# Kernel optimization log

Hardware: AMD Instinct MI355X
Metric: run time of the kernel (lower is better)

Reference implementation:

```python
import jax, jax.numpy as jnp
import numpy as np

D_MODEL = 512
D_INNER = 1024      # expand * d_model
NHEADS = 16         # d_inner // headdim, headdim = d_model // num_heads = 64
HEADDIM = 64
DSTATE = 64
DCONV = 4           # window_size
DFF = 2048
B, LM, LT = 16, 1024, 512


def _rmsnorm(x, eps=1e-6):
    return x * jax.lax.rsqrt(jnp.mean(x * x, axis=-1, keepdims=True) + eps)


def setup_inputs():
    key = jax.random.key(0)
    ks = jax.random.split(key, 10)
    conv_dim = D_INNER + 2 * DSTATE
    d_in_proj = 2 * D_INNER + 2 * DSTATE + NHEADS
    return {
        'tgt': jax.random.normal(ks[0], (B, LT, D_MODEL), jnp.float32),
        'memory': jax.random.normal(ks[1], (B, LM, D_MODEL), jnp.float32),
        'mem_mask': jnp.ones((B, LM), jnp.float32),
        'tgt_mask': jnp.ones((B, LT), jnp.float32),
        'in_proj_w': jax.random.normal(ks[2], (d_in_proj, D_MODEL), jnp.float32) * 0.02,
        'conv_w': jax.random.normal(ks[3], (conv_dim, DCONV), jnp.float32) * 0.2,
        'conv_b': jnp.zeros((conv_dim,), jnp.float32),
        'dt_bias': jax.random.uniform(ks[4], (NHEADS,), jnp.float32, -4.0, -2.0),
        'A_log': jnp.log(jax.random.uniform(ks[5], (NHEADS,), jnp.float32, 1.0, 16.0)),
        'D': jnp.ones((NHEADS,), jnp.float32),
        'norm_w': jnp.ones((D_INNER,), jnp.float32),
        'out_proj_w': jax.random.normal(ks[6], (D_MODEL, D_INNER), jnp.float32) * 0.02,
        'fc1_w': jax.random.normal(ks[7], (DFF, D_MODEL), jnp.float32) * 0.02,
        'fc1_b': jnp.zeros((DFF,), jnp.float32),
        'fc2_w': jax.random.normal(ks[8], (D_MODEL, DFF), jnp.float32) * 0.02,
        'fc2_b': jnp.zeros((D_MODEL,), jnp.float32),
    }


def _mamba2(u, in_proj_w, conv_w, conv_b, dt_bias, A_log, D, norm_w, out_proj_w):
    # u: (B, L, d_model) -- Mamba2-style selective scan (causal, ngroups=1)
    b, L, _ = u.shape
    zxbcdt = jnp.einsum('bld,ed->ble', u, in_proj_w)  # (B,L,2192)
    z = zxbcdt[..., :D_INNER]
    xBC = zxbcdt[..., D_INNER:D_INNER + D_INNER + 2 * DSTATE]
    dt = zxbcdt[..., -NHEADS:]

    # causal depthwise conv1d, kernel = DCONV, then swish
    xBC_pad = jnp.pad(xBC, ((0, 0), (DCONV - 1, 0), (0, 0)))
    conv = conv_b
    conv = sum(conv_w[:, k] * xBC_pad[:, k:k + L] for k in range(DCONV)) + conv_b
    xBC = jax.nn.silu(conv)

    x = xBC[..., :D_INNER].reshape(b, L, NHEADS, HEADDIM)   # (B,L,H,P)
    Bm = xBC[..., D_INNER:D_INNER + DSTATE]                  # (B,L,N)
    Cm = xBC[..., D_INNER + DSTATE:]                         # (B,L,N)

    dt = jax.nn.softplus(dt + dt_bias)                       # (B,L,H)
    A = -jnp.exp(A_log)                                      # (H,)
    a = jnp.exp(dt * A)                                      # (B,L,H) decay

    def step(h, inputs):
        a_t, dt_t, x_t, B_t, C_t = inputs
        # h: (B,H,P,N)
        h = a_t[:, :, None, None] * h + (dt_t[:, :, None] * x_t)[..., None] * B_t[:, None, None, :]
        y = jnp.einsum('bhpn,bn->bhp', h, C_t)
        return h, y

    h0 = jnp.zeros((b, NHEADS, HEADDIM, DSTATE), u.dtype)
    xs = (jnp.moveaxis(a, 1, 0), jnp.moveaxis(dt, 1, 0), jnp.moveaxis(x, 1, 0),
          jnp.moveaxis(Bm, 1, 0), jnp.moveaxis(Cm, 1, 0))
    _, ys = jax.lax.scan(step, h0, xs)                       # (L,B,H,P)
    y = jnp.moveaxis(ys, 0, 1) + D[None, None, :, None] * x  # skip term
    y = y.reshape(b, L, D_INNER)

    # gated RMSNorm + out_proj
    y = y * jax.nn.silu(z)
    y = _rmsnorm(y, 1e-5) * norm_w
    return jnp.einsum('ble,de->bld', y, out_proj_w)


def _forward(tgt, memory, mem_mask, tgt_mask, in_proj_w, conv_w, conv_b, dt_bias,
             A_log, D, norm_w, out_proj_w, fc1_w, fc1_b, fc2_w, fc2_b):
    tgt = tgt * tgt_mask[..., None]
    tgt1 = _rmsnorm(tgt)
    memory = memory * mem_mask[..., None]
    u = jnp.concatenate([memory, tgt1], axis=1)
    mask = jnp.concatenate([mem_mask, tgt_mask], axis=1)
    u = u * mask[..., None]
    tgt2 = _mamba2(u, in_proj_w, conv_w, conv_b, dt_bias, A_log, D, norm_w, out_proj_w)
    tgt2 = tgt2[:, -tgt1.shape[1]:]
    tgt = tgt + tgt2  # dropout = identity (eval)
    tgt1 = _rmsnorm(tgt)
    h = jax.nn.gelu(jnp.einsum('bld,fd->blf', tgt1, fc1_w) + fc1_b, approximate=False)
    tgt2 = jnp.einsum('blf,df->bld', h, fc2_w) + fc2_b
    return tgt + tgt2


def reference(tgt, memory, mem_mask, tgt_mask, in_proj_w, conv_w, conv_b, dt_bias,
              A_log, D, norm_w, out_proj_w, fc1_w, fc1_b, fc2_w, fc2_b):
    return _forward(tgt, memory, mem_mask, tgt_mask, in_proj_w, conv_w, conv_b, dt_bias,
                    A_log, D, norm_w, out_proj_w, fc1_w, fc1_b, fc2_w, fc2_b)
```

## Files before the change

kernel.cpp:

```cpp
#include <hip/hip_runtime.h>
#include <cstddef>

#define BB 16
#define LMM 1024
#define LTT 512
#define LL 1536
#define DMODEL 512
#define DINNER 1024
#define NH 16
#define DIPROJ 2192
#define DFF2 2048

typedef __bf16 bf16_t;
typedef bf16_t bf16x2 __attribute__((ext_vector_type(2)));
typedef bf16_t bf16x4 __attribute__((ext_vector_type(4)));
typedef bf16_t bf16x8 __attribute__((ext_vector_type(8)));
typedef float f32x4 __attribute__((ext_vector_type(4)));

typedef __attribute__((address_space(3))) void lds_void;
typedef const __attribute__((address_space(1))) void glb_void;

__device__ __forceinline__ void gload16(const void* g, void* l) {
  __builtin_amdgcn_global_load_lds((glb_void*)g, (lds_void*)l, 16, 0, 0);
}

__device__ inline float block_sum(float v, float* sbuf) {
#pragma unroll
  for (int off = 32; off > 0; off >>= 1) v += __shfl_xor(v, off, 64);
  int w = threadIdx.x >> 6;
  if ((threadIdx.x & 63) == 0) sbuf[w] = v;
  __syncthreads();
  return sbuf[0] + sbuf[1] + sbuf[2] + sbuf[3];
}

__global__ __launch_bounds__(256)
void cvt_w(const float* __restrict__ src, bf16_t* __restrict__ dst, int n)
{
  int i = (blockIdx.x * 256 + threadIdx.x) * 4;
  if (i < n) {
    float4 v = *(const float4*)&src[i];
    bf16x4 o;
    o[0] = (bf16_t)v.x; o[1] = (bf16_t)v.y; o[2] = (bf16_t)v.z; o[3] = (bf16_t)v.w;
    *(bf16x4*)&dst[i] = o;
  }
}

__global__ __launch_bounds__(256)
void prep_u(const float* __restrict__ tgt, const float* __restrict__ memory,
            const float* __restrict__ mem_mask, const float* __restrict__ tgt_mask,
            bf16_t* __restrict__ u, float* __restrict__ tgtm)
{
  __shared__ float sbuf[4];
  const int row = blockIdx.x;
  const int b = row / LL;
  const int t = row - b * LL;
  const int tid = threadIdx.x;
  if (t < LMM) {
    float m = mem_mask[b * LMM + t];
    float s = m * m;
    const float* src = memory + ((size_t)b * LMM + t) * DMODEL;
    float2 v = *(const float2*)&src[tid * 2];
    bf16x2 o; o[0] = (bf16_t)(v.x * s); o[1] = (bf16_t)(v.y * s);
    *(bf16x2*)&u[(size_t)row * DMODEL + tid * 2] = o;
  } else {
    const int tt = t - LMM;
    float mk = tgt_mask[b * LTT + tt];
    const float* src = tgt + ((size_t)b * LTT + tt) * DMODEL;
    float2 v = *(const float2*)&src[tid * 2];
    v.x *= mk; v.y *= mk;
    *(float2*)&tgtm[((size_t)b * LTT + tt) * DMODEL + tid * 2] = v;
    float ss = block_sum(v.x * v.x + v.y * v.y, sbuf);
    float inv = rsqrtf(ss * (1.0f / 512.0f) + 1e-6f) * mk;
    bf16x2 o; o[0] = (bf16_t)(v.x * inv); o[1] = (bf16_t)(v.y * inv);
    *(bf16x2*)&u[(size_t)row * DMODEL + tid * 2] = o;
  }
}

template<int EPI>
__global__ __launch_bounds__(256)
void gemm_abf(const bf16_t* __restrict__ A, const bf16_t* __restrict__ W,
              int M, int N, int K,
              float* __restrict__ Cf, bf16_t* __restrict__ Cb,
              const float* __restrict__ bias, const float* __restrict__ res,
              bf16_t* __restrict__ zbuf, bf16_t* __restrict__ xbc,
              float* __restrict__ dts, float* __restrict__ labuf,
              const float* __restrict__ dt_bias, const float* __restrict__ A_log)
{
  const int m0 = blockIdx.y * 128;
  const int n0 = blockIdx.x * 128;
  int bq = 0, tbase = 0;
  if (EPI == 4) {
    bq = m0 / LL; tbase = m0 - bq * LL;
    if (n0 + 128 <= DINNER && tbase < LMM) return;
  }
  __shared__ __align__(16) bf16_t As[128 * 64];
  __shared__ __align__(16) bf16_t Bs[128 * 64];
  const int tid = threadIdx.x;
  const int lane = tid & 63;
  const int wid = tid >> 6;
  const int wr = (wid >> 1) * 64, wc = (wid & 1) * 64;
  const int r = lane & 15;
  const int g = lane >> 4;
  const int r7 = r & 7;
  const int lrow = lane >> 3;
  const int sslot = (lane & 7) ^ lrow;

  int arow[4], brow[4];
#pragma unroll
  for (int ci = 0; ci < 4; ++ci) {
    int tr = wid * 32 + ci * 8 + lrow;
    arow[ci] = m0 + tr;
    int bn = n0 + tr;
    brow[ci] = bn < N ? bn : N - 1;
  }

  f32x4 acc[4][4];
#pragma unroll
  for (int m = 0; m < 4; ++m)
#pragma unroll
    for (int n = 0; n < 4; ++n) acc[m][n] = (f32x4){0.f, 0.f, 0.f, 0.f};

  for (int kt = 0; kt < K; kt += 64) {
#pragma unroll
    for (int ci = 0; ci < 4; ++ci) {
      int chunk = wid * 4 + ci;
      gload16(A + (size_t)arow[ci] * K + kt + sslot * 8, &As[chunk * 512]);
      gload16(W + (size_t)brow[ci] * K + kt + sslot * 8, &Bs[chunk * 512]);
    }
    __syncthreads();
#pragma unroll
    for (int c = 0; c < 2; ++c) {
      bf16x8 af[4], bfr[4];
#pragma unroll
      for (int m = 0; m < 4; ++m) {
        int row = wr + m * 16 + r;
        af[m] = *(const bf16x8*)&As[row * 64 + (((c * 4 + g) ^ r7) * 8)];
      }
#pragma unroll
      for (int n = 0; n < 4; ++n) {
        int row = wc + n * 16 + r;
        bfr[n] = *(const bf16x8*)&Bs[row * 64 + (((c * 4 + g) ^ r7) * 8)];
      }
#pragma unroll
      for (int m = 0; m < 4; ++m)
#pragma unroll
        for (int n = 0; n < 4; ++n)
          acc[m][n] = __builtin_amdgcn_mfma_f32_16x16x32_bf16(af[m], bfr[n], acc[m][n], 0, 0, 0);
    }
    __syncthreads();
  }

#pragma unroll
  for (int m = 0; m < 4; ++m) {
#pragma unroll
    for (int n = 0; n < 4; ++n) {
      int gcol = n0 + wc + n * 16 + r;
      if (gcol >= N) continue;
#pragma unroll
      for (int j = 0; j < 4; ++j) {
        float v = acc[m][n][j];
        if (EPI == 4) {
          int t = tbase + wr + m * 16 + g * 4 + j;
          if (gcol < DINNER) {
            zbuf[(((size_t)(bq * LTT + t - LMM)) << 10) + gcol] = (bf16_t)v;
          } else if (gcol < DINNER + 1152) {
            xbc[(size_t)(bq * LL + t) * 1152 + (gcol - DINNER)] = (bf16_t)v;
          } else {
            int h = gcol - 2176;
            float raw = v + dt_bias[h];
            float d = raw > 20.f ? raw : log1pf(expf(raw));
            size_t ix = (size_t)(bq * LL + t) * 16 + h;
            dts[ix] = d;
            labuf[ix] = -expf(A_log[h]) * d;
          }
        } else {
          int grow = m0 + wr + m * 16 + g * 4 + j;
          if (EPI == 1) {
            v += bias[gcol];
            v = 0.5f * v * (1.f + erff(v * 0.70710678f));
            Cb[(size_t)grow * N + gcol] = (bf16_t)v;
          } else if (EPI == 2) {
            v += bias[gcol] + res[(size_t)grow * N + gcol];
            Cf[(size_t)grow * N + gcol] = v;
          } else {
            v += res[(size_t)grow * N + gcol];
            Cf[(size_t)grow * N + gcol] = v;
          }
        }
      }
    }
  }
}

__global__ __launch_bounds__(256)
void sbc_k(const bf16_t* __restrict__ xbc, const float* __restrict__ cw,
           const float* __restrict__ cb, bf16_t* __restrict__ BtG,
           bf16_t* __restrict__ Sg, bf16_t* __restrict__ CcG)
{
  __shared__ __align__(16) bf16_t rawBC[132 * 128];
  __shared__ __align__(16) bf16_t CB[128 * 128];
  __shared__ float wls[128 * 4];
  __shared__ float bls[128];
  const int c = blockIdx.x, b = blockIdx.y;
  const int t0 = c * 128;
  const int tid = threadIdx.x, lane = tid & 63, wid = tid >> 6;
  const int r = lane & 15, g = lane >> 4;

  if (tid < 128) {
    int gch = 1024 + tid;
#pragma unroll
    for (int k = 0; k < 4; ++k) wls[tid * 4 + k] = cw[gch * 4 + k];
    bls[tid] = cb[gch];
  }
#pragma unroll
  for (int ci = 0; ci < 9; ++ci) {
    int chunk = ci * 4 + wid;
    if (chunk < 33) {
      int F = chunk * 1024 + lane * 16;
      int row = F >> 8, off = F & 255;
      gload16(xbc + (size_t)(b * LL + t0 - 3 + row) * 1152 + 1024 + off / 2,
              &rawBC[chunk * 512]);
    }
  }
  __syncthreads();
  if (c == 0 && tid < 48) {
    bf16x8 z; 
#pragma unroll
    for (int j = 0; j < 8; ++j) z[j] = (bf16_t)0.f;
    *(bf16x8*)&rawBC[tid * 8] = z;
  }
  __syncthreads();
#pragma unroll 2
  for (int it = 0; it < 64; ++it) {
    int o = tid + it * 256;
    int t = o >> 7, ch = o & 127;
    float a0 = bls[ch];
#pragma unroll
    for (int kk = 0; kk < 4; ++kk)
      a0 = fmaf(wls[ch * 4 + kk], (float)rawBC[(t + kk) * 128 + ch], a0);
    float sv = a0 / (1.f + expf(-a0));
    int slot = ch >> 3;
    int swslot = (slot & 8) | ((slot & 7) ^ (t & 7));
    CB[t * 128 + swslot * 8 + (ch & 7)] = (bf16_t)sv;
    if (c >= 8 && ch >= 64) {
      int n = ch - 64;
      CcG[(((size_t)(b * 4 + (c - 8)) * 128 + t)) * 64 + (((n >> 3) ^ (t & 7)) << 3) + (n & 7)] = (bf16_t)sv;
    }
  }
  __syncthreads();
  {
    int n = tid & 63, tb = tid >> 6;
#pragma unroll
    for (int s8 = 0; s8 < 4; ++s8) {
      int ts = tb * 32 + s8 * 8;
      bf16x8 v;
#pragma unroll
      for (int e = 0; e < 8; ++e) {
        int t = ts + e;
        int slot = (n >> 3) ^ (t & 7);
        v[e] = CB[t * 128 + slot * 8 + (n & 7)];
      }
      *(bf16x8*)&BtG[((size_t)(b * 12 + c) * 64 + n) * 128 + ((((ts >> 3) ^ (n & 7))) << 3)] = v;
    }
  }
  if (c >= 8) {
    f32x4 sacc[2][8];
#pragma unroll
    for (int tt = 0; tt < 2; ++tt)
#pragma unroll
      for (int ct = 0; ct < 8; ++ct) sacc[tt][ct] = (f32x4){0.f, 0.f, 0.f, 0.f};
    const int ctn = 2 * wid + 2;
#pragma unroll
    for (int kk = 0; kk < 2; ++kk) {
      bf16x8 ca[2];
#pragma unroll
      for (int tt = 0; tt < 2; ++tt) {
        int trow = wid * 32 + tt * 16 + r;
        int slot = (64 + kk * 32 + g * 8) >> 3;
        int sw = (slot & 8) | ((slot & 7) ^ (trow & 7));
        ca[tt] = *(const bf16x8*)&CB[trow * 128 + sw * 8];
      }
#pragma unroll
      for (int ct = 0; ct < 8; ++ct) {
        if (ct < ctn) {
          int taur = ct * 16 + r;
          int sw = ((kk * 4 + g) ^ (taur & 7));
          bf16x8 bb = *(const bf16x8*)&CB[taur * 128 + sw * 8];
          sacc[0][ct] = __builtin_amdgcn_mfma_f32_16x16x32_bf16(ca[0], bb, sacc[0][ct], 0, 0, 0);
          sacc[1][ct] = __builtin_amdgcn_mfma_f32_16x16x32_bf16(ca[1], bb, sacc[1][ct], 0, 0, 0);
        }
      }
    }
    size_t sbase = (size_t)(b * 4 + (c - 8)) * 16384;
#pragma unroll
    for (int tt = 0; tt < 2; ++tt)
#pragma unroll
      for (int ct = 0; ct < 8; ++ct) {
        if (ct < ctn) {
#pragma unroll
          for (int j = 0; j < 4; ++j) {
            int ta = wid * 32 + tt * 16 + g * 4 + j;
            int tau = ct * 16 + r;
            Sg[sbase + ta * 128 + (tau ^ ((ta & 7) << 3))] = (bf16_t)sacc[tt][ct][j];
          }
        }
      }
  }
}

__global__ __launch_bounds__(256)
void ssd_hend(const bf16_t* __restrict__ xbc, const float* __restrict__ dts,
              const float* __restrict__ labuf, const float* __restrict__ cw,
              const float* __restrict__ cb, const bf16_t* __restrict__ BtG,
              bf16_t* __restrict__ hend, float* __restrict__ Lacum,
              float* __restrict__ Ak)
{
  __shared__ __align__(16) bf16_t rawX[136 * 64];
  __shared__ __align__(16) bf16_t Xt[64 * 128];
  __shared__ __align__(16) bf16_t Bt[64 * 128];
  __shared__ float wv[128];
  __shared__ float wls[64 * 4];
  __shared__ float bls[64];
  const int c = blockIdx.x;
  const int bh = blockIdx.y;
  const int b = bh >> 4, h = bh & 15;
  const int t0 = c * 128;
  const int tid = threadIdx.x, lane = tid & 63, wid = tid >> 6;
  const int r = lane & 15, g = lane >> 4;

  if (tid < 64) {
    int gch = h * 64 + tid;
#pragma unroll
    for (int k = 0; k < 4; ++k) wls[tid * 4 + k] = cw[gch * 4 + k];
    bls[tid] = cb[gch];
  }
#pragma unroll
  for (int ci = 0; ci < 5; ++ci) {
    int chunk = ci * 4 + wid;
    if (chunk < 17) {
      int F = chunk * 1024 + lane * 16;
      int row = F >> 7, off = F & 127;
      gload16(xbc + (size_t)(b * LL + t0 - 3 + row) * 1152 + h * 64 + off / 2,
              &rawX[chunk * 512]);
    }
  }
#pragma unroll
  for (int ci = 0; ci < 4; ++ci) {
    int chunk = ci * 4 + wid;
    int F = chunk * 1024 + lane * 16;
    gload16(BtG + (size_t)(b * 12 + c) * 8192 + F / 2, &Bt[chunk * 512]);
  }
  __syncthreads();
  if (c == 0 && tid < 24) {
    bf16x8 z;
#pragma unroll
    for (int j = 0; j < 8; ++j) z[j] = (bf16_t)0.f;
    *(bf16x8*)&rawX[tid * 8] = z;
  }
  if (tid < 64) {
    float v0 = labuf[(size_t)(b * LL + t0 + tid) * 16 + h];
    float v1 = labuf[(size_t)(b * LL + t0 + 64 + tid) * 16 + h];
    float d0 = dts[(size_t)(b * LL + t0 + tid) * 16 + h];
    float d1 = dts[(size_t)(b * LL + t0 + 64 + tid) * 16 + h];
#pragma unroll
    for (int d = 1; d < 64; d <<= 1) { float t_ = __shfl(v0, tid - d, 64); if (tid >= d) v0 += t_; }
    float T0 = __shfl(v0, 63, 64);
#pragma unroll
    for (int d = 1; d < 64; d <<= 1) { float t_ = __shfl(v1, tid - d, 64); if (tid >= d) v1 += t_; }
    v1 += T0;
    float Ls = __shfl(v1, 63, 64);
    wv[tid] = expf(Ls - v0) * d0; wv[64 + tid] = expf(Ls - v1) * d1;
    Lacum[(size_t)(bh * 12 + c) * 128 + tid] = v0;
    Lacum[(size_t)(bh * 12 + c) * 128 + 64 + tid] = v1;
    if (tid == 0) Ak[bh * 12 + c] = expf(Ls);
  }
  __syncthreads();
  {
    int p = tid & 63, tb = (tid >> 6) * 32;
    float w0 = wls[p * 4], w1 = wls[p * 4 + 1], w2 = wls[p * 4 + 2], w3 = wls[p * 4 + 3];
    float bb0 = bls[p];
    int sw = (p & 7) << 3;
#pragma unroll
    for (int i8 = 0; i8 < 4; ++i8) {
      bf16x8 ov;
#pragma unroll
      for (int e = 0; e < 8; ++e) {
        int t = tb + i8 * 8 + e;
        float a0 = bb0;
        a0 = fmaf(w0, (float)rawX[(t + 0) * 64 + p], a0);
        a0 = fmaf(w1, (float)rawX[(t + 1) * 64 + p], a0);
        a0 = fmaf(w2, (float)rawX[(t + 2) * 64 + p], a0);
        a0 = fmaf(w3, (float)rawX[(t + 3) * 64 + p], a0);
        ov[e] = (bf16_t)(a0 / (1.f + expf(-a0)));
      }
      *(bf16x8*)&Xt[p * 128 + ((tb + i8 * 8) ^ sw)] = ov;
    }
  }
  __syncthreads();
  f32x4 acc[4];
#pragma unroll
  for (int n = 0; n < 4; ++n) acc[n] = (f32x4){0.f, 0.f, 0.f, 0.f};
  const int prow = wid * 16 + r;
#pragma unroll
  for (int kk = 0; kk < 4; ++kk) {
    int k0 = kk * 32 + g * 8;
    bf16x8 xv = *(const bf16x8*)&Xt[prow * 128 + (k0 ^ ((prow & 7) << 3))];
    bf16x8 af;
#pragma unroll
    for (int j = 0; j < 8; ++j) af[j] = (bf16_t)((float)xv[j] * wv[k0 + j]);
#pragma unroll
    for (int nt = 0; nt < 4; ++nt) {
      int nrow = nt * 16 + r;
      bf16x8 bf_ = *(const bf16x8*)&Bt[nrow * 128 + (k0 ^ ((nrow & 7) << 3))];
      acc[nt] = __builtin_amdgcn_mfma_f32_16x16x32_bf16(af, bf_, acc[nt], 0, 0, 0);
    }
  }
  size_t base = ((size_t)(bh * 12 + c)) * 4096;
#pragma unroll
  for (int nt = 0; nt < 4; ++nt)
#pragma unroll
    for (int j = 0; j < 4; ++j)
      hend[base + (size_t)(wid * 16 + g * 4 + j) * 64 + nt * 16 + r] = (bf16_t)acc[nt][j];
}

__global__ __launch_bounds__(256)
void ssd_y(const bf16_t* __restrict__ xbc, const float* __restrict__ dts,
           const bf16_t* __restrict__ hend, const float* __restrict__ Ak,
           const float* __restrict__ Lacum, const bf16_t* __restrict__ Sg,
           const bf16_t* __restrict__ CcG, const float* __restrict__ cw,
           const float* __restrict__ cb, const float* __restrict__ Dp,
           bf16_t* __restrict__ ybuf)
{
  __shared__ __align__(16) char region0[32768];
  __shared__ __align__(16) bf16_t Xt[64 * 128];
  __shared__ __align__(16) bf16_t Cs[128 * 64];
  __shared__ __align__(16) bf16_t hts[64 * 64];
  __shared__ float Lat[128];
  __shared__ float dtv[128];
  __shared__ float wls[64 * 4];
  __shared__ float bls[64];
  bf16_t* rawX = (bf16_t*)region0;
  bf16_t* Gs   = (bf16_t*)region0;
  const int c = 8 + blockIdx.x;
  const int bh = blockIdx.y;
  const int b = bh >> 4, h = bh & 15;
  const int t0 = c * 128;
  const int tid = threadIdx.x, lane = tid & 63, wid = tid >> 6;
  const int r = lane & 15, g = lane >> 4;

  if (tid < 64) {
    int gch = h * 64 + tid;
#pragma unroll
    for (int k = 0; k < 4; ++k) wls[tid * 4 + k] = cw[gch * 4 + k];
    bls[tid] = cb[gch];
  }
  if (tid < 128) {
    Lat[tid] = Lacum[(size_t)(bh * 12 + c) * 128 + tid];
    dtv[tid] = dts[(size_t)(b * LL + t0 + tid) * 16 + h];
  }
#pragma unroll
  for (int ci = 0; ci < 5; ++ci) {
    int chunk = ci * 4 + wid;
    if (chunk < 17) {
      int F = chunk * 1024 + lane * 16;
      int row = F >> 7, off = F & 127;
      gload16(xbc + (size_t)(b * LL + t0 - 3 + row) * 1152 + h * 64 + off / 2,
              &rawX[chunk * 512]);
    }
  }
#pragma unroll
  for (int ci = 0; ci < 4; ++ci) {
    int chunk = ci * 4 + wid;
    int F = chunk * 1024 + lane * 16;
    gload16(CcG + (size_t)(b * 4 + (c - 8)) * 8192 + F / 2, &Cs[chunk * 512]);
  }
  {
    float hin[16];
#pragma unroll
    for (int e = 0; e < 16; ++e) hin[e] = 0.f;
    float accp = 1.f;
    for (int k = c - 1; k >= 0; --k) {
      const bf16_t* hp = hend + ((size_t)(bh * 12 + k)) * 4096 + tid * 16;
      bf16x8 e0 = *(const bf16x8*)hp;
      bf16x8 e1 = *(const bf16x8*)(hp + 8);
#pragma unroll
      for (int j = 0; j < 8; ++j) {
        hin[j]     = fmaf(accp, (float)e0[j], hin[j]);
        hin[j + 8] = fmaf(accp, (float)e1[j], hin[j + 8]);
      }
      accp *= Ak[bh * 12 + k];
    }
    int p = tid >> 2, n0 = (tid & 3) * 16;
    bf16x8 o0, o1;
#pragma unroll
    for (int j = 0; j < 8; ++j) { o0[j] = (bf16_t)hin[j]; o1[j] = (bf16_t)hin[j + 8]; }
    int p7 = p & 7;
    *(bf16x8*)&hts[p * 64 + (((n0 >> 3) ^ p7) << 3)] = o0;
    *(bf16x8*)&hts[p * 64 + ((((n0 >> 3) + 1) ^ p7) << 3)] = o1;
  }
  __syncthreads();
  {
    int p = tid & 63, tb = (tid >> 6) * 32;
    float w0 = wls[p * 4], w1 = wls[p * 4 + 1], w2 = wls[p * 4 + 2], w3 = wls[p * 4 + 3];
    float bb0 = bls[p];
    int sw = (p & 7) << 3;
#pragma unroll
    for (int i8 = 0; i8 < 4; ++i8) {
      bf16x8 ov;
#pragma unroll
      for (int e = 0; e < 8; ++e) {
        int t = tb + i8 * 8 + e;
        float a0 = bb0;
        a0 = fmaf(w0, (float)rawX[(t + 0) * 64 + p], a0);
        a0 = fmaf(w1, (float)rawX[(t + 1) * 64 + p], a0);
        a0 = fmaf(w2, (float)rawX[(t + 2) * 64 + p], a0);
        a0 = fmaf(w3, (float)rawX[(t + 3) * 64 + p], a0);
        ov[e] = (bf16_t)(a0 / (1.f + expf(-a0)));
      }
      *(bf16x8*)&Xt[p * 128 + ((tb + i8 * 8) ^ sw)] = ov;
    }
  }
  __syncthreads();
  {
    size_t sbase = (size_t)(b * 4 + (c - 8)) * 16384;
#pragma unroll
    for (int it = 0; it < 8; ++it) {
      int o = tid + it * 256;
      int ta = o >> 4, sl = o & 15;
      bf16x8 sv = *(const bf16x8*)&Sg[sbase + ta * 128 + sl * 8];
      int tau0 = (sl ^ (ta & 7)) * 8;
      float Lta = Lat[ta];
      bf16x8 gv;
#pragma unroll
      for (int e = 0; e < 8; ++e) {
        int tau = tau0 + e;
        float xa = (tau <= ta) ? (Lta - Lat[tau]) : -1e30f;
        gv[e] = (bf16_t)(expf(xa) * dtv[tau] * (float)sv[e]);
      }
      *(bf16x8*)&Gs[ta * 128 + sl * 8] = gv;
    }
  }
  __syncthreads();

  bf16x8 caf[2][2];
#pragma unroll
  for (int tt = 0; tt < 2; ++tt)
#pragma unroll
    for (int kk = 0; kk < 2; ++kk) {
      int trow = wid * 32 + tt * 16 + r;
      caf[tt][kk] = *(const bf16x8*)&Cs[trow * 64 + ((((kk * 4 + g)) ^ (trow & 7)) << 3)];
    }

  f32x4 accY[2][4], acc2[2][4];
#pragma unroll
  for (int tt = 0; tt < 2; ++tt)
#pragma unroll
    for (int pt = 0; pt < 4; ++pt) {
      accY[tt][pt] = (f32x4){0.f, 0.f, 0.f, 0.f};
      acc2[tt][pt] = (f32x4){0.f, 0.f, 0.f, 0.f};
    }
#pragma unroll
  for (int tt = 0; tt < 2; ++tt) {
    int trow = wid * 32 + tt * 16 + r;
#pragma unroll
    for (int kk = 0; kk < 4; ++kk) {
      if (kk <= wid) {
        int k0 = kk * 32 + g * 8;
        bf16x8 ga = *(const bf16x8*)&Gs[trow * 128 + (k0 ^ ((trow & 7) << 3))];
#pragma unroll
        for (int pt = 0; pt < 4; ++pt) {
          int prow = pt * 16 + r;
          bf16x8 xb = *(const bf16x8*)&Xt[prow * 128 + (k0 ^ ((prow & 7) << 3))];
          accY[tt][pt] = __builtin_amdgcn_mfma_f32_16x16x32_bf16(ga, xb, accY[tt][pt], 0, 0, 0);
        }
      }
    }
#pragma unroll
    for (int kk = 0; kk < 2; ++kk) {
#pragma unroll
      for (int pt = 0; pt < 4; ++pt) {
        int prow = pt * 16 + r;
        bf16x8 hb = *(const bf16x8*)&hts[prow * 64 + ((((kk * 4 + g)) ^ (prow & 7)) << 3)];
        acc2[tt][pt] = __builtin_amdgcn_mfma_f32_16x16x32_bf16(caf[tt][kk], hb, acc2[tt][pt], 0, 0, 0);
      }
    }
  }

  const float Dh = Dp[h];
#pragma unroll
  for (int tt = 0; tt < 2; ++tt) {
#pragma unroll
    for (int j = 0; j < 4; ++j) {
      int trow = wid * 32 + tt * 16 + g * 4 + j;
      float el = expf(Lat[trow]);
      size_t yrow = ((size_t)(b * LTT + (c - 8) * 128 + trow)) << 10;
#pragma unroll
      for (int pt = 0; pt < 4; ++pt) {
        int p = pt * 16 + r;
        float xv = (float)Xt[p * 128 + (trow ^ ((p & 7) << 3))];
        float yv = accY[tt][pt][j] + el * acc2[tt][pt][j] + Dh * xv;
        ybuf[yrow + h * 64 + p] = (bf16_t)yv;
      }
    }
  }
}

__global__ __launch_bounds__(256)
void gate_norm_k(const bf16_t* __restrict__ zbuf, const bf16_t* __restrict__ ybuf,
                 const float* __restrict__ norm_w, bf16_t* __restrict__ yn)
{
  __shared__ float sbuf[4];
  const int row = blockIdx.x;
  const int tid = threadIdx.x;
  bf16x4 yv = *(const bf16x4*)&ybuf[(size_t)row * DINNER + tid * 4];
  bf16x4 zv = *(const bf16x4*)&zbuf[(size_t)row * DINNER + tid * 4];
  float v[4];
#pragma unroll
  for (int c = 0; c < 4; ++c) {
    float y = (float)yv[c], z = (float)zv[c];
    v[c] = y * (z / (1.f + expf(-z)));
  }
  float ss = block_sum(v[0]*v[0] + v[1]*v[1] + v[2]*v[2] + v[3]*v[3], sbuf);
  float inv = rsqrtf(ss * (1.f / 1024.f) + 1e-5f);
  float4 nw = *(const float4*)&norm_w[tid * 4];
  bf16x4 o;
  o[0] = (bf16_t)(v[0] * inv * nw.x); o[1] = (bf16_t)(v[1] * inv * nw.y);
  o[2] = (bf16_t)(v[2] * inv * nw.z); o[3] = (bf16_t)(v[3] * inv * nw.w);
  *(bf16x4*)&yn[(size_t)row * DINNER + tid * 4] = o;
}

__global__ __launch_bounds__(256)
void rms_k(const float* __restrict__ in, bf16_t* __restrict__ out)
{
  __shared__ float sbuf[4];
  const int row = blockIdx.x;
  const int tid = threadIdx.x;
  float2 v = *(const float2*)&in[(size_t)row * DMODEL + tid * 2];
  float ss = block_sum(v.x * v.x + v.y * v.y, sbuf);
  float inv = rsqrtf(ss * (1.f / 512.f) + 1e-6f);
  bf16x2 o; o[0] = (bf16_t)(v.x * inv); o[1] = (bf16_t)(v.y * inv);
  *(bf16x2*)&out[(size_t)row * DMODEL + tid * 2] = o;
}

extern "C" void kernel_launch(void* const* d_in, const int* in_sizes, int n_in,
                              void* d_out, int out_size, void* d_ws, size_t ws_size,
                              hipStream_t stream)
{
  const float* tgt        = (const float*)d_in[0];
  const float* memory     = (const float*)d_in[1];
  const float* mem_mask   = (const float*)d_in[2];
  const float* tgt_mask   = (const float*)d_in[3];
  const float* in_proj_w  = (const float*)d_in[4];
  const float* conv_w     = (const float*)d_in[5];
  const float* conv_b     = (const float*)d_in[6];
  const float* dt_bias    = (const float*)d_in[7];
  const float* A_log      = (const float*)d_in[8];
  const float* Dp         = (const float*)d_in[9];
  const float* norm_w     = (const float*)d_in[10];
  const float* out_proj_w = (const float*)d_in[11];
  const float* fc1_w      = (const float*)d_in[12];
  const float* fc1_b      = (const float*)d_in[13];
  const float* fc2_w      = (const float*)d_in[14];
  const float* fc2_b      = (const float*)d_in[15];

  char* wsb = (char*)d_ws;
  bf16_t* u     = (bf16_t*)(wsb + 0);
  bf16_t* zbuf  = (bf16_t*)(wsb + 25165824);
  bf16_t* xbc   = (bf16_t*)(wsb + 41943040);
  float*  dts   = (float*)(wsb + 98566144);
  float*  labuf = (float*)(wsb + 100139008);
  float*  tgtm  = (float*)(wsb + 101711872);
  bf16_t* hend  = (bf16_t*)(wsb + 118489088);
  float*  Lacum = (float*)(wsb + 143667200);
  float*  Akb   = (float*)(wsb + 145240064);
  bf16_t* BtG   = (bf16_t*)(wsb + 145252352);
  bf16_t* Sg    = (bf16_t*)(wsb + 148398080);
  bf16_t* CcG   = (bf16_t*)(wsb + 150495232);
  bf16_t* wip   = (bf16_t*)(wsb + 160444416);
  bf16_t* wop   = wip + 1122304;
  bf16_t* wf1   = wop + 524288;
  bf16_t* wf2   = wf1 + 1048576;
  bf16_t* ybuf  = (bf16_t*)(wsb + 0);
  bf16_t* yn    = (bf16_t*)(wsb + 41943040);
  float*  tres  = (float*)(wsb + 58720256);
  bf16_t* t1    = (bf16_t*)(wsb + 75497472);
  bf16_t* hbuf  = (bf16_t*)(wsb + 0);
  float* outp = (float*)d_out;

  cvt_w<<<1096, 256, 0, stream>>>(in_proj_w, wip, 1122304);
  cvt_w<<<512, 256, 0, stream>>>(out_proj_w, wop, 524288);
  cvt_w<<<1024, 256, 0, stream>>>(fc1_w, wf1, 1048576);
  cvt_w<<<1024, 256, 0, stream>>>(fc2_w, wf2, 1048576);
  prep_u<<<BB * LL, 256, 0, stream>>>(tgt, memory, mem_mask, tgt_mask, u, tgtm);
  gemm_abf<4><<<dim3(18, 192), 256, 0, stream>>>(u, wip, BB * LL, DIPROJ, DMODEL,
      nullptr, nullptr, nullptr, nullptr, zbuf, xbc, dts, labuf, dt_bias, A_log);
  sbc_k<<<dim3(12, BB), 256, 0, stream>>>(xbc, conv_w, conv_b, BtG, Sg, CcG);
  ssd_hend<<<dim3(12, BB * NH), 256, 0, stream>>>(xbc, dts, labuf, conv_w, conv_b,
      BtG, hend, Lacum, Akb);
  ssd_y<<<dim3(4, BB * NH), 256, 0, stream>>>(xbc, dts, hend, Akb, Lacum, Sg, CcG,
      conv_w, conv_b, Dp, ybuf);
  gate_norm_k<<<BB * LTT, 256, 0, stream>>>(zbuf, ybuf, norm_w, yn);
  gemm_abf<3><<<dim3(4, 64), 256, 0, stream>>>(yn, wop, BB * LTT, DMODEL, DINNER,
      tres, nullptr, nullptr, tgtm, nullptr, nullptr, nullptr, nullptr, nullptr, nullptr);
  rms_k<<<BB * LTT, 256, 0, stream>>>(tres, t1);
  gemm_abf<1><<<dim3(16, 64), 256, 0, stream>>>(t1, wf1, BB * LTT, DFF2, DMODEL,
      nullptr, hbuf, fc1_b, nullptr, nullptr, nullptr, nullptr, nullptr, nullptr, nullptr);
  gemm_abf<2><<<dim3(4, 64), 256, 0, stream>>>(hbuf, wf2, BB * LTT, DMODEL, DFF2,
      outp, nullptr, fc2_b, tres, nullptr, nullptr, nullptr, nullptr, nullptr, nullptr);
}
```

Measured before the change: 336.3 us.

## Double-buffer GEMM LDS tiles and swizzle workgroup order across XCDs

The bf16 GEMM kernel now keeps two LDS buffers for the A and W tiles. It issues the global-to-LDS loads for the next K tile before running the MFMAs on the current one, which removes one barrier per iteration and overlaps load latency with compute. It also remaps the flat block index so that consecutive workgroups are spread in groups of eight, aiming for better L2 locality across the chiplets. This doubles LDS use to 64KB per block, which may lower occupancy, and the swizzle assumes the workgroup count divides evenly by eight.

```diff
diff --git a/kernel.cpp b/kernel.cpp
--- a/kernel.cpp
+++ b/kernel.cpp
@@ -86,15 +86,19 @@
               float* __restrict__ dts, float* __restrict__ labuf,
               const float* __restrict__ dt_bias, const float* __restrict__ A_log)
 {
-  const int m0 = blockIdx.y * 128;
-  const int n0 = blockIdx.x * 128;
+  const int nbx = gridDim.x;
+  const int nwg = nbx * gridDim.y;
+  int flat = blockIdx.y * nbx + blockIdx.x;
+  int swz = (flat & 7) * (nwg >> 3) + (flat >> 3);
+  const int m0 = (swz / nbx) * 128;
+  const int n0 = (swz % nbx) * 128;
   int bq = 0, tbase = 0;
   if (EPI == 4) {
     bq = m0 / LL; tbase = m0 - bq * LL;
     if (n0 + 128 <= DINNER && tbase < LMM) return;
   }
-  __shared__ __align__(16) bf16_t As[128 * 64];
-  __shared__ __align__(16) bf16_t Bs[128 * 64];
+  __shared__ __align__(16) bf16_t As[2][128 * 64];
+  __shared__ __align__(16) bf16_t Bs[2][128 * 64];
   const int tid = threadIdx.x;
   const int lane = tid & 63;
   const int wid = tid >> 6;
@@ -114,32 +118,39 @@
     brow[ci] = bn < N ? bn : N - 1;
   }
 
-  f32x4 acc[4][4];
-#pragma unroll
-  for (int m = 0; m < 4; ++m)
-#pragma unroll
-    for (int n = 0; n < 4; ++n) acc[m][n] = (f32x4){0.f, 0.f, 0.f, 0.f};
-
-  for (int kt = 0; kt < K; kt += 64) {
+  auto stage = [&](int buf, int kt) {
 #pragma unroll
     for (int ci = 0; ci < 4; ++ci) {
       int chunk = wid * 4 + ci;
-      gload16(A + (size_t)arow[ci] * K + kt + sslot * 8, &As[chunk * 512]);
-      gload16(W + (size_t)brow[ci] * K + kt + sslot * 8, &Bs[chunk * 512]);
-    }
-    __syncthreads();
+      gload16(A + (size_t)arow[ci] * K + kt + sslot * 8, &As[buf][chunk * 512]);
+      gload16(W + (size_t)brow[ci] * K + kt + sslot * 8, &Bs[buf][chunk * 512]);
+    }
+  };
+
+  f32x4 acc[4][4];
+#pragma unroll
+  for (int m = 0; m < 4; ++m)
+#pragma unroll
+    for (int n = 0; n < 4; ++n) acc[m][n] = (f32x4){0.f, 0.f, 0.f, 0.f};
+
+  const int NK = K >> 6;
+  stage(0, 0);
+  __syncthreads();
+  for (int ki = 0; ki < NK; ++ki) {
+    const int cur = ki & 1;
+    if (ki + 1 < NK) stage(cur ^ 1, (ki + 1) << 6);
 #pragma unroll
     for (int c = 0; c < 2; ++c) {
       bf16x8 af[4], bfr[4];
 #pragma unroll
       for (int m = 0; m < 4; ++m) {
         int row = wr + m * 16 + r;
-        af[m] = *(const bf16x8*)&As[row * 64 + (((c * 4 + g) ^ r7) * 8)];
+        af[m] = *(const bf16x8*)&As[cur][row * 64 + (((c * 4 + g) ^ r7) * 8)];
       }
 #pragma unroll
       for (int n = 0; n < 4; ++n) {
         int row = wc + n * 16 + r;
-        bfr[n] = *(const bf16x8*)&Bs[row * 64 + (((c * 4 + g) ^ r7) * 8)];
+        bfr[n] = *(const bf16x8*)&Bs[cur][row * 64 + (((c * 4 + g) ^ r7) * 8)];
       }
 #pragma unroll
       for (int m = 0; m < 4; ++m)
@@ -147,7 +158,7 @@
         for (int n = 0; n < 4; ++n)
           acc[m][n] = __builtin_amdgcn_mfma_f32_16x16x32_bf16(af[m], bfr[n], acc[m][n], 0, 0, 0);
     }
-    __syncthreads();
+    if (ki + 1 < NK) __syncthreads();
   }
 
 #pragma unroll
@@ -224,7 +235,7 @@
   }
   __syncthreads();
   if (c == 0 && tid < 48) {
-    bf16x8 z; 
+    bf16x8 z;
 #pragma unroll
     for (int j = 0; j < 8; ++j) z[j] = (bf16_t)0.f;
     *(bf16x8*)&rawBC[tid * 8] = z;
```

After: 338.6 us. Within noise of the previous version (+0.7%).

## Add 256x128 tile GEMM for in_proj and fc1, swizzle blocks, merge weight casts

Applied to the files above, without the earlier changes.

Introduces a 512-thread GEMM with 256-row M tiles for the in_proj and fc1 projections, halving the grid and raising weight-tile reuse per block. Both GEMM kernels now remap block IDs with an XCD-style swizzle so neighbouring tiles share cache. The four weight conversion launches become one kernel. The larger tile reduces the in_proj early-exit skip granularity for memory rows, and larger blocks may cut occupancy.

```diff
diff --git a/kernel.cpp b/kernel.cpp
--- a/kernel.cpp
+++ b/kernel.cpp
@@ -34,15 +34,22 @@
 }
 
 __global__ __launch_bounds__(256)
-void cvt_w(const float* __restrict__ src, bf16_t* __restrict__ dst, int n)
+void cvt_all(const float* __restrict__ s0, const float* __restrict__ s1,
+             const float* __restrict__ s2, const float* __restrict__ s3,
+             bf16_t* __restrict__ dst)
 {
   int i = (blockIdx.x * 256 + threadIdx.x) * 4;
-  if (i < n) {
-    float4 v = *(const float4*)&src[i];
-    bf16x4 o;
-    o[0] = (bf16_t)v.x; o[1] = (bf16_t)v.y; o[2] = (bf16_t)v.z; o[3] = (bf16_t)v.w;
-    *(bf16x4*)&dst[i] = o;
-  }
+  if (i >= 3743744) return;
+  const float* src;
+  int off;
+  if (i < 1122304)      { src = s0; off = i; }
+  else if (i < 1646592) { src = s1; off = i - 1122304; }
+  else if (i < 2695168) { src = s2; off = i - 1646592; }
+  else                  { src = s3; off = i - 2695168; }
+  float4 v = *(const float4*)&src[off];
+  bf16x4 o;
+  o[0] = (bf16_t)v.x; o[1] = (bf16_t)v.y; o[2] = (bf16_t)v.z; o[3] = (bf16_t)v.w;
+  *(bf16x4*)&dst[i] = o;
 }
 
 __global__ __launch_bounds__(256)
@@ -80,19 +87,15 @@
 __global__ __launch_bounds__(256)
 void gemm_abf(const bf16_t* __restrict__ A, const bf16_t* __restrict__ W,
               int M, int N, int K,
-              float* __restrict__ Cf, bf16_t* __restrict__ Cb,
-              const float* __restrict__ bias, const float* __restrict__ res,
-              bf16_t* __restrict__ zbuf, bf16_t* __restrict__ xbc,
-              float* __restrict__ dts, float* __restrict__ labuf,
-              const float* __restrict__ dt_bias, const float* __restrict__ A_log)
-{
-  const int m0 = blockIdx.y * 128;
-  const int n0 = blockIdx.x * 128;
-  int bq = 0, tbase = 0;
-  if (EPI == 4) {
-    bq = m0 / LL; tbase = m0 - bq * LL;
-    if (n0 + 128 <= DINNER && tbase < LMM) return;
-  }
+              float* __restrict__ Cf, const float* __restrict__ bias,
+              const float* __restrict__ res)
+{
+  const int nbx = gridDim.x;
+  const int nwg = nbx * gridDim.y;
+  int flat = blockIdx.y * nbx + blockIdx.x;
+  int swz = (flat & 7) * (nwg >> 3) + (flat >> 3);
+  const int m0 = (swz / nbx) * 128;
+  const int n0 = (swz % nbx) * 128;
   __shared__ __align__(16) bf16_t As[128 * 64];
   __shared__ __align__(16) bf16_t Bs[128 * 64];
   const int tid = threadIdx.x;
@@ -159,10 +162,108 @@
 #pragma unroll
       for (int j = 0; j < 4; ++j) {
         float v = acc[m][n][j];
+        int grow = m0 + wr + m * 16 + g * 4 + j;
+        if (EPI == 2) v += bias[gcol] + res[(size_t)grow * N + gcol];
+        else          v += res[(size_t)grow * N + gcol];
+        Cf[(size_t)grow * N + gcol] = v;
+      }
+    }
+  }
+}
+
+template<int EPI>
+__global__ __launch_bounds__(512)
+void gemm_big(const bf16_t* __restrict__ A, const bf16_t* __restrict__ W,
+              int M, int N, int K,
+              bf16_t* __restrict__ Cb, const float* __restrict__ bias,
+              bf16_t* __restrict__ zbuf, bf16_t* __restrict__ xbc,
+              float* __restrict__ dts, float* __restrict__ labuf,
+              const float* __restrict__ dt_bias, const float* __restrict__ A_log)
+{
+  const int nbx = gridDim.x;
+  const int nwg = nbx * gridDim.y;
+  int flat = blockIdx.y * nbx + blockIdx.x;
+  int swz = (flat & 7) * (nwg >> 3) + (flat >> 3);
+  const int m0 = (swz / nbx) * 256;
+  const int n0 = (swz % nbx) * 128;
+  int bq = 0, tbase = 0;
+  if (EPI == 4) {
+    bq = m0 / LL; tbase = m0 - bq * LL;
+    if (n0 + 128 <= DINNER && tbase + 256 <= LMM) return;
+  }
+  __shared__ __align__(16) bf16_t As[256 * 64];
+  __shared__ __align__(16) bf16_t Bs[128 * 64];
+  const int tid = threadIdx.x;
+  const int lane = tid & 63;
+  const int wid = tid >> 6;
+  const int wr = (wid >> 1) * 64;
+  const int wc = (wid & 1) * 64;
+  const int r = lane & 15;
+  const int g = lane >> 4;
+  const int r7 = r & 7;
+  const int lrow = lane >> 3;
+  const int sslot = (lane & 7) ^ lrow;
+
+  int arow[4], brow[2];
+#pragma unroll
+  for (int ci = 0; ci < 4; ++ci) arow[ci] = m0 + wid * 32 + ci * 8 + lrow;
+#pragma unroll
+  for (int ci = 0; ci < 2; ++ci) {
+    int bn = n0 + wid * 16 + ci * 8 + lrow;
+    brow[ci] = bn < N ? bn : N - 1;
+  }
+
+  f32x4 acc[4][4];
+#pragma unroll
+  for (int m = 0; m < 4; ++m)
+#pragma unroll
+    for (int n = 0; n < 4; ++n) acc[m][n] = (f32x4){0.f, 0.f, 0.f, 0.f};
+
+  for (int kt = 0; kt < K; kt += 64) {
+#pragma unroll
+    for (int ci = 0; ci < 4; ++ci)
+      gload16(A + (size_t)arow[ci] * K + kt + sslot * 8, &As[(wid * 4 + ci) * 512]);
+#pragma unroll
+    for (int ci = 0; ci < 2; ++ci)
+      gload16(W + (size_t)brow[ci] * K + kt + sslot * 8, &Bs[(wid * 2 + ci) * 512]);
+    __syncthreads();
+#pragma unroll
+    for (int c = 0; c < 2; ++c) {
+      bf16x8 af[4], bfr[4];
+#pragma unroll
+      for (int m = 0; m < 4; ++m) {
+        int row = wr + m * 16 + r;
+        af[m] = *(const bf16x8*)&As[row * 64 + (((c * 4 + g) ^ r7) * 8)];
+      }
+#pragma unroll
+      for (int n = 0; n < 4; ++n) {
+        int row = wc + n * 16 + r;
+        bfr[n] = *(const bf16x8*)&Bs[row * 64 + (((c * 4 + g) ^ r7) * 8)];
+      }
+#pragma unroll
+      for (int m = 0; m < 4; ++m)
+#pragma unroll
+        for (int n = 0; n < 4; ++n)
+          acc[m][n] = __builtin_amdgcn_mfma_f32_16x16x32_bf16(af[m], bfr[n], acc[m][n], 0, 0, 0);
+    }
+    __syncthreads();
+  }
+
+#pragma unroll
+  for (int m = 0; m < 4; ++m) {
+#pragma unroll
+    for (int n = 0; n < 4; ++n) {
+      int gcol = n0 + wc + n * 16 + r;
+      if (gcol >= N) continue;
+#pragma unroll
+      for (int j = 0; j < 4; ++j) {
+        float v = acc[m][n][j];
+        int lrow2 = wr + m * 16 + g * 4 + j;
         if (EPI == 4) {
-          int t = tbase + wr + m * 16 + g * 4 + j;
+          int t = tbase + lrow2;
           if (gcol < DINNER) {
-            zbuf[(((size_t)(bq * LTT + t - LMM)) << 10) + gcol] = (bf16_t)v;
+            if (t >= LMM)
+              zbuf[(((size_t)(bq * LTT + t - LMM)) << 10) + gcol] = (bf16_t)v;
           } else if (gcol < DINNER + 1152) {
             xbc[(size_t)(bq * LL + t) * 1152 + (gcol - DINNER)] = (bf16_t)v;
           } else {
@@ -174,18 +275,10 @@
             labuf[ix] = -expf(A_log[h]) * d;
           }
         } else {
-          int grow = m0 + wr + m * 16 + g * 4 + j;
-          if (EPI == 1) {
-            v += bias[gcol];
-            v = 0.5f * v * (1.f + erff(v * 0.70710678f));
-            Cb[(size_t)grow * N + gcol] = (bf16_t)v;
-          } else if (EPI == 2) {
-            v += bias[gcol] + res[(size_t)grow * N + gcol];
-            Cf[(size_t)grow * N + gcol] = v;
-          } else {
-            v += res[(size_t)grow * N + gcol];
-            Cf[(size_t)grow * N + gcol] = v;
-          }
+          int grow = m0 + lrow2;
+          v += bias[gcol];
+          v = 0.5f * v * (1.f + erff(v * 0.70710678f));
+          Cb[(size_t)grow * N + gcol] = (bf16_t)v;
         }
       }
     }
@@ -224,7 +317,7 @@
   }
   __syncthreads();
   if (c == 0 && tid < 48) {
-    bf16x8 z; 
+    bf16x8 z;
 #pragma unroll
     for (int j = 0; j < 8; ++j) z[j] = (bf16_t)0.f;
     *(bf16x8*)&rawBC[tid * 8] = z;
@@ -687,13 +780,10 @@
   bf16_t* hbuf  = (bf16_t*)(wsb + 0);
   float* outp = (float*)d_out;
 
-  cvt_w<<<1096, 256, 0, stream>>>(in_proj_w, wip, 1122304);
-  cvt_w<<<512, 256, 0, stream>>>(out_proj_w, wop, 524288);
-  cvt_w<<<1024, 256, 0, stream>>>(fc1_w, wf1, 1048576);
-  cvt_w<<<1024, 256, 0, stream>>>(fc2_w, wf2, 1048576);
+  cvt_all<<<3656, 256, 0, stream>>>(in_proj_w, out_proj_w, fc1_w, fc2_w, wip);
   prep_u<<<BB * LL, 256, 0, stream>>>(tgt, memory, mem_mask, tgt_mask, u, tgtm);
-  gemm_abf<4><<<dim3(18, 192), 256, 0, stream>>>(u, wip, BB * LL, DIPROJ, DMODEL,
-      nullptr, nullptr, nullptr, nullptr, zbuf, xbc, dts, labuf, dt_bias, A_log);
+  gemm_big<4><<<dim3(18, 96), 512, 0, stream>>>(u, wip, BB * LL, DIPROJ, DMODEL,
+      nullptr, nullptr, zbuf, xbc, dts, labuf, dt_bias, A_log);
   sbc_k<<<dim3(12, BB), 256, 0, stream>>>(xbc, conv_w, conv_b, BtG, Sg, CcG);
   ssd_hend<<<dim3(12, BB * NH), 256, 0, stream>>>(xbc, dts, labuf, conv_w, conv_b,
       BtG, hend, Lacum, Akb);
@@ -701,10 +791,10 @@
       conv_w, conv_b, Dp, ybuf);
   gate_norm_k<<<BB * LTT, 256, 0, stream>>>(zbuf, ybuf, norm_w, yn);
   gemm_abf<3><<<dim3(4, 64), 256, 0, stream>>>(yn, wop, BB * LTT, DMODEL, DINNER,
-      tres, nullptr, nullptr, tgtm, nullptr, nullptr, nullptr, nullptr, nullptr, nullptr);
+      tres, nullptr, tgtm);
   rms_k<<<BB * LTT, 256, 0, stream>>>(tres, t1);
-  gemm_abf<1><<<dim3(16, 64), 256, 0, stream>>>(t1, wf1, BB * LTT, DFF2, DMODEL,
-      nullptr, hbuf, fc1_b, nullptr, nullptr, nullptr, nullptr, nullptr, nullptr, nullptr);
+  gemm_big<1><<<dim3(16, 32), 512, 0, stream>>>(t1, wf1, BB * LTT, DFF2, DMODEL,
+      hbuf, fc1_b, nullptr, nullptr, nullptr, nullptr, nullptr, nullptr);
   gemm_abf<2><<<dim3(4, 64), 256, 0, stream>>>(hbuf, wf2, BB * LTT, DMODEL, DFF2,
-      outp, nullptr, fc2_b, tres, nullptr, nullptr, nullptr, nullptr, nullptr, nullptr);
-}
+      outp, fc2_b, tres);
+}
```

Result: faster. 301.5 us, median of 2 (-10.4%).
